# Performance work log

Measured on AMD Instinct MI355X. Metric: run time of the kernel, lower is better.

The kernel has to match this reference:

```python
import jax, jax.numpy as jnp
import numpy as np

D, NH, E, F = 768, 12, 4, 3072            # embed dim, heads, experts/group, expert ffn (4*D)
NBLK, DEPTH = 2, 6                        # MoE blocks, DiT depth
N_A, N_B, N_C = 64, 32, 192               # group token counts
MA, FH, TC = 32, 8, 7                     # max_agents, future_horizon, traj_channels
BATCH = 8
T_TRAJ = MA * FH                          # 256 trajectory tokens
TFREQ = 256                               # sinusoidal timestep embedding dim
HD = D // NH

def _ln(x):
    mu = jnp.mean(x, -1, keepdims=True)
    v = jnp.var(x, -1, keepdims=True)
    return (x - mu) * jax.lax.rsqrt(v + 1e-6)

def _heads(x):
    b, n, _ = x.shape
    return x.reshape(b, n, NH, HD).transpose(0, 2, 1, 3)

def _attn(q, k, v):
    s = jnp.einsum('bhqd,bhkd->bhqk', q, k) * (HD ** -0.5)
    p = jax.nn.softmax(s, -1)
    o = jnp.einsum('bhqk,bhkd->bhqd', p, v)
    b, h, n, d = o.shape
    return o.transpose(0, 2, 1, 3).reshape(b, n, h * d)

def _cross(q_in, kv_in, W):
    # W: [4, D, D] = (Wq, Wk, Wv, Wo)
    q = _heads(q_in @ W[0]); k = _heads(kv_in @ W[1]); v = _heads(kv_in @ W[2])
    return _attn(q, k, v) @ W[3]

def _moe(x, Wr, W1, W2):
    # top-1 switch routing: gate = softmax prob of selected expert
    gates = jax.nn.softmax(x @ Wr)                       # [B,N,E]
    idx = jnp.argmax(gates, -1)                          # [B,N]
    gval = jnp.take_along_axis(gates, idx[..., None], -1)  # [B,N,1]
    h = jax.nn.gelu(jnp.einsum('bnd,edf->bnef', x, W1))
    y = jnp.einsum('bnef,efd->bned', h, W2)
    sel = jax.nn.one_hot(idx, W1.shape[0], dtype=x.dtype) * gval
    return jnp.einsum('bned,bne->bnd', y, sel)

def _forward(x_traj, tokens_A, tokens_B, tokens_C, W_traj, b_traj, W_ftime,
             Wt1, bt1, Wt2, bt2, moe_attn_W, moe_router, moe_W1, moe_W2,
             dit_qkv, dit_qkv_b, dit_proj, dit_proj_b, dit_mlp1, dit_mlp1_b,
             dit_mlp2, dit_mlp2_b, dit_ada, dit_ada_b,
             out_ada_W, out_ada_b, out_W, out_b, t):
    B = x_traj.shape[0]
    # timestep conditioning (DiT TimestepEmbedder)
    half = TFREQ // 2
    freqs = jnp.exp(-np.log(10000.0) * jnp.arange(half, dtype=jnp.float32) / half)
    ang = t.astype(jnp.float32)[:, None] * freqs
    temb = jnp.concatenate([jnp.cos(ang), jnp.sin(ang)], -1)     # [B,TFREQ]
    c = jax.nn.silu(temb @ Wt1 + bt1) @ Wt2 + bt2                # [B,D]

    # trajectory embedding + future-time embedding
    traj = x_traj.reshape(B, T_TRAJ, TC) @ W_traj + b_traj       # [B,256,D]
    traj = traj + jnp.tile(W_ftime, (MA, 1))[None]

    # StackedMoEBlocks: directed cross-attn A->C->B + per-group top-1 expert routing
    a, bg, cg = tokens_A, tokens_B, tokens_C
    for i in range(NBLK):
        cg = cg + _cross(_ln(cg), a, moe_attn_W[i, 0])
        bg = bg + _cross(_ln(bg), cg, moe_attn_W[i, 1])
        a = a + _moe(_ln(a), moe_router[i, 0], moe_W1[i, 0], moe_W2[i, 0])
        bg = bg + _moe(_ln(bg), moe_router[i, 1], moe_W1[i, 1], moe_W2[i, 1])
        cg = cg + _moe(_ln(cg), moe_router[i, 2], moe_W1[i, 2], moe_W2[i, 2])

    # DiT backbone over [traj | A | B | C], adaLN-zero conditioning on c
    x = jnp.concatenate([traj, a, bg, cg], 1)                    # [B,544,D]
    for i in range(DEPTH):
        mod = (jax.nn.silu(c) @ dit_ada[i] + dit_ada_b[i]).reshape(B, 6, 1, D)
        s1, sc1, g1, s2, sc2, g2 = [mod[:, j] for j in range(6)]
        h = _ln(x) * (1 + sc1) + s1
        qkv = h @ dit_qkv[i] + dit_qkv_b[i]
        q, k, v = jnp.split(qkv, 3, -1)
        x = x + g1 * (_attn(_heads(q), _heads(k), _heads(v)) @ dit_proj[i] + dit_proj_b[i])
        h = _ln(x) * (1 + sc2) + s2
        x = x + g2 * (jax.nn.gelu(h @ dit_mlp1[i] + dit_mlp1_b[i]) @ dit_mlp2[i] + dit_mlp2_b[i])

    # output head: final adaLN + projection to noise(+sigma), trajectory tokens only
    shift, scale = jnp.split(jax.nn.silu(c) @ out_ada_W + out_ada_b, 2, -1)
    h = _ln(x) * (1 + scale[:, None]) + shift[:, None]
    out = h @ out_W + out_b
    return out[:, :T_TRAJ].reshape(B, MA, FH, 2 * TC)

def setup_inputs() -> dict:
    key = jax.random.key(0)
    ks = jax.random.split(key, 24)
    n = jax.random.normal
    s = 0.02
    return dict(
        x_traj=n(ks[0], (BATCH, MA, FH, TC), jnp.float32),
        t=jax.random.randint(ks[1], (BATCH,), 0, 50),
        tokens_A=n(ks[2], (BATCH, N_A, D), jnp.float32),
        tokens_B=n(ks[3], (BATCH, N_B, D), jnp.float32),
        tokens_C=n(ks[4], (BATCH, N_C, D), jnp.float32),
        W_traj=n(ks[5], (TC, D)) * s, b_traj=jnp.zeros((D,)),
        W_ftime=n(ks[6], (FH, D)) * s,
        Wt1=n(ks[7], (TFREQ, D)) * s, bt1=jnp.zeros((D,)),
        Wt2=n(ks[8], (D, D)) * s, bt2=jnp.zeros((D,)),
        moe_attn_W=n(ks[9], (NBLK, 2, 4, D, D)) * s,
        moe_router=n(ks[10], (NBLK, 3, D, E)) * s,
        moe_W1=n(ks[11], (NBLK, 3, E, D, F)) * s,
        moe_W2=n(ks[12], (NBLK, 3, E, F, D)) * s,
        dit_qkv=n(ks[13], (DEPTH, D, 3 * D)) * s, dit_qkv_b=jnp.zeros((DEPTH, 3 * D)),
        dit_proj=n(ks[14], (DEPTH, D, D)) * s, dit_proj_b=jnp.zeros((DEPTH, D)),
        dit_mlp1=n(ks[15], (DEPTH, D, 4 * D)) * s, dit_mlp1_b=jnp.zeros((DEPTH, 4 * D)),
        dit_mlp2=n(ks[16], (DEPTH, 4 * D, D)) * s, dit_mlp2_b=jnp.zeros((DEPTH, D)),
        dit_ada=n(ks[17], (DEPTH, D, 6 * D)) * s, dit_ada_b=jnp.zeros((DEPTH, 6 * D)),
        out_ada_W=n(ks[18], (D, 2 * D)) * s, out_ada_b=jnp.zeros((2 * D,)),
        out_W=n(ks[19], (D, 2 * TC)) * s, out_b=jnp.zeros((2 * TC,)),
    )

def reference(x_traj, t, tokens_A, tokens_B, tokens_C, W_traj, b_traj, W_ftime,
              Wt1, bt1, Wt2, bt2, moe_attn_W, moe_router, moe_W1, moe_W2,
              dit_qkv, dit_qkv_b, dit_proj, dit_proj_b, dit_mlp1, dit_mlp1_b,
              dit_mlp2, dit_mlp2_b, dit_ada, dit_ada_b,
              out_ada_W, out_ada_b, out_W, out_b):
    return _forward(x_traj, tokens_A, tokens_B, tokens_C, W_traj, b_traj, W_ftime,
                    Wt1, bt1, Wt2, bt2, moe_attn_W, moe_router, moe_W1, moe_W2,
                    dit_qkv, dit_qkv_b, dit_proj, dit_proj_b, dit_mlp1, dit_mlp1_b,
                    dit_mlp2, dit_mlp2_b, dit_ada, dit_ada_b,
                    out_ada_W, out_ada_b, out_W, out_b, t)
```

## Files before the change

kernel.cpp:

```cpp
#include <hip/hip_runtime.h>
#include <hip/hip_bf16.h>
#include <math.h>

#define D 768
#define NH 12
#define HD 64
#define NEXP 4
#define FF 3072
#define NBLK 2
#define DEPTH 6
#define NA 64
#define NB 32
#define NC 192
#define BATCH 8
#define TTRAJ 256
#define NTOK 544
#define MAXTOK 1536
#define MOER 2304

typedef __attribute__((ext_vector_type(8))) short short8v;
typedef __attribute__((ext_vector_type(4))) float f32x4;

__device__ __forceinline__ float siluf(float v) { return v / (1.f + expf(-v)); }
__device__ __forceinline__ float geluf(float v) {
    float u = 0.7978845608028654f * (v + 0.044715f * v * v * v);
    return 0.5f * v * (1.f + tanhf(u));
}
__device__ __forceinline__ unsigned short f2bf(float f) {
    union { float f; unsigned u; } v; v.f = f;
    unsigned r = v.u + 0x7fffu + ((v.u >> 16) & 1u);
    return (unsigned short)(r >> 16);
}
__device__ __forceinline__ float bf2f(unsigned short u) {
    union { unsigned u; float f; } v; v.u = ((unsigned)u) << 16; return v.f;
}
__device__ __forceinline__ void gl16(const unsigned short* g, unsigned short* l) {
    __builtin_amdgcn_global_load_lds(
        (const __attribute__((address_space(1))) void*)g,
        (__attribute__((address_space(3))) void*)l, 16, 0, 0);
}

__global__ void timestep_kernel(const int* __restrict__ t, unsigned short* __restrict__ tembP) {
    int i = blockIdx.x * blockDim.x + threadIdx.x;
    if (i >= 128 * 256) return;
    int b = i >> 8, j = i & 255;
    float v = 0.f;
    if (b < BATCH) {
        int jj = (j & 127);
        float freq = expf(-logf(10000.f) * (float)jj / 128.f);
        float ang = (float)t[b] * freq;
        v = (j < 128) ? cosf(ang) : sinf(ang);
    }
    tembP[i] = f2bf(v);
}

__global__ void add_ftime(float* __restrict__ traj, const float* __restrict__ wf, int total) {
    int i = blockIdx.x * blockDim.x + threadIdx.x;
    if (i >= total) return;
    int col = i % D;
    int n = (i / D) % TTRAJ;
    traj[i] += wf[(n & 7) * D + col];
}

__global__ void cvt_bf16(const float* __restrict__ in, unsigned short* __restrict__ out, int n8) {
    int i = blockIdx.x * blockDim.x + threadIdx.x;
    if (i >= n8) return;
    float4 a = *(const float4*)(in + i * 8);
    float4 b = *(const float4*)(in + i * 8 + 4);
    unsigned short t[8] = {f2bf(a.x), f2bf(a.y), f2bf(a.z), f2bf(a.w),
                           f2bf(b.x), f2bf(b.y), f2bf(b.z), f2bf(b.w)};
    *(short8v*)(out + i * 8) = *(short8v*)t;
}

template<int ACT>
__global__ __launch_bounds__(256) void gemm_act(
    const float* __restrict__ A, int lda,
    const float* __restrict__ B, int ldb,
    const float* __restrict__ bias,
    float* __restrict__ C, int ldc,
    int M, int N, int K)
{
    __shared__ float As[16][65];
    __shared__ float Bs[16][65];
    int tid = threadIdx.x;
    int tx = tid & 15, ty = tid >> 4;
    int row0 = blockIdx.y * 64, col0 = blockIdx.x * 64;
    float acc[4][4] = {};
    for (int k0 = 0; k0 < K; k0 += 16) {
        #pragma unroll
        for (int i = 0; i < 4; ++i) {
            int e = tid + 256 * i; int m = e >> 4; int kk = e & 15;
            int gr = row0 + m, gk = k0 + kk;
            As[kk][m] = (gr < M && gk < K) ? A[(size_t)gr * lda + gk] : 0.f;
        }
        #pragma unroll
        for (int i = 0; i < 4; ++i) {
            int e = tid + 256 * i; int kk = e >> 6; int n = e & 63;
            int gk = k0 + kk, gc = col0 + n;
            Bs[kk][n] = (gk < K && gc < N) ? B[(size_t)gk * ldb + gc] : 0.f;
        }
        __syncthreads();
        #pragma unroll
        for (int kk = 0; kk < 16; ++kk) {
            float a[4], bv[4];
            #pragma unroll
            for (int i = 0; i < 4; ++i) a[i] = As[kk][ty * 4 + i];
            #pragma unroll
            for (int j = 0; j < 4; ++j) bv[j] = Bs[kk][tx * 4 + j];
            #pragma unroll
            for (int i = 0; i < 4; ++i)
                #pragma unroll
                for (int j = 0; j < 4; ++j) acc[i][j] += a[i] * bv[j];
        }
        __syncthreads();
    }
    #pragma unroll
    for (int i = 0; i < 4; ++i) {
        int gr = row0 + ty * 4 + i; if (gr >= M) continue;
        #pragma unroll
        for (int j = 0; j < 4; ++j) {
            int gc = col0 + tx * 4 + j; if (gc >= N) continue;
            float v = acc[i][j] + (bias ? bias[gc] : 0.f);
            if (ACT == 1) v = siluf(v);
            if (ACT == 2) v = geluf(v);
            C[(size_t)gr * ldc + gc] = v;
        }
    }
}

__global__ __launch_bounds__(256) void transpose_cvt(
    const float* __restrict__ in, unsigned short* __restrict__ out, int K, int N)
{
    __shared__ unsigned short Ls[64][72];
    const float* src = in + (size_t)blockIdx.z * K * N;
    unsigned short* dst = out + (size_t)blockIdx.z * K * N;
    int k0 = blockIdx.y * 64, n0 = blockIdx.x * 64;
    int tid = threadIdx.x;
    int r = tid >> 2, c0 = (tid & 3) * 16;
    {
        const float* sp = src + (size_t)(k0 + r) * N + n0 + c0;
        #pragma unroll
        for (int j = 0; j < 16; j += 4) {
            float4 f = *(const float4*)(sp + j);
            Ls[c0 + j + 0][r] = f2bf(f.x);
            Ls[c0 + j + 1][r] = f2bf(f.y);
            Ls[c0 + j + 2][r] = f2bf(f.z);
            Ls[c0 + j + 3][r] = f2bf(f.w);
        }
    }
    __syncthreads();
    {
        unsigned short tmp[16];
        #pragma unroll
        for (int j = 0; j < 16; ++j) tmp[j] = Ls[r][c0 + j];
        unsigned short* dp = dst + (size_t)(n0 + r) * K + k0 + c0;
        *(short8v*)dp = *(short8v*)tmp;
        *(short8v*)(dp + 8) = *(short8v*)(tmp + 8);
    }
}

template<int ACT, int OUT, int TN, int TM>
__global__ __launch_bounds__(256) void gemm_lds(
    const unsigned short* __restrict__ A,
    const unsigned short* __restrict__ BT,
    const float* __restrict__ bias,
    float* __restrict__ Cf, unsigned short* __restrict__ Cb, int ldc,
    int K, int qscale_cols,
    const float* __restrict__ mod, int modstride, int gchunk, int ntok, int mrows,
    size_t bt_zs = 0, size_t bias_zs = 0, size_t c_zs = 0)
{
    constexpr int NCF = TN / 32;
    constexpr int NBS = TN / 64;
    constexpr int NMR = TM / 32;
    constexpr int NAI = TM / 64;
    constexpr int NST = (NAI > NBS) ? NAI : NBS;
    if (bt_zs) BT += (size_t)blockIdx.z * bt_zs;
    if (bias && bias_zs) bias += (size_t)blockIdx.z * bias_zs;
    if (c_zs) { if (Cf) Cf += (size_t)blockIdx.z * c_zs; if (Cb) Cb += (size_t)blockIdx.z * c_zs; }
    __shared__ unsigned short As[2][TM * 32];
    __shared__ unsigned short Bs[2][TN * 32];
    int tid = threadIdx.x, w = tid >> 6, lane = tid & 63;
    int row0 = blockIdx.y * TM, col0 = blockIdx.x * TN;
    int wrow = (w >> 1) * (TM / 2), wcol = (w & 1) * (TN / 2);
    int lr = lane & 15, g = lane >> 4;
    f32x4 acc[NMR][NCF] = {};

    int ra[NST], ka[NST], la[NST];
    #pragma unroll
    for (int i = 0; i < NST; ++i) {
        int off = tid * 16 + i * 4096;
        int row = off >> 6;
        int slot = (off >> 4) & 3;
        ra[i] = row;
        ka[i] = (slot ^ ((row >> 1) & 3)) * 8;
        la[i] = off >> 1;
    }
    int nt = K >> 5, cur = 0;
    #pragma unroll
    for (int i = 0; i < NAI; ++i)
        gl16(A + (size_t)(row0 + ra[i]) * K + ka[i], &As[0][la[i]]);
    #pragma unroll
    for (int i = 0; i < NBS; ++i)
        gl16(BT + (size_t)(col0 + ra[i]) * K + ka[i], &Bs[0][la[i]]);

    for (int t = 0; t < nt; ++t) {
        __syncthreads();
        if (t + 1 < nt) {
            int k0 = (t + 1) << 5;
            #pragma unroll
            for (int i = 0; i < NAI; ++i)
                gl16(A + (size_t)(row0 + ra[i]) * K + k0 + ka[i], &As[cur ^ 1][la[i]]);
            #pragma unroll
            for (int i = 0; i < NBS; ++i)
                gl16(BT + (size_t)(col0 + ra[i]) * K + k0 + ka[i], &Bs[cur ^ 1][la[i]]);
        }
        short8v av[NMR], bv[NCF];
        #pragma unroll
        for (int mr = 0; mr < NMR; ++mr) {
            int row = wrow + mr * 16 + lr;
            av[mr] = *(const short8v*)&As[cur][row * 32 + (g ^ ((row >> 1) & 3)) * 8];
        }
        #pragma unroll
        for (int nc = 0; nc < NCF; ++nc) {
            int row = wcol + nc * 16 + lr;
            bv[nc] = *(const short8v*)&Bs[cur][row * 32 + (g ^ ((row >> 1) & 3)) * 8];
        }
        #pragma unroll
        for (int mr = 0; mr < NMR; ++mr)
            #pragma unroll
            for (int nc = 0; nc < NCF; ++nc)
                acc[mr][nc] = __builtin_amdgcn_mfma_f32_16x16x32_bf16(
                    av[mr], bv[nc], acc[mr][nc], 0, 0, 0);
        cur ^= 1;
    }
    int rbase = g * 4;
    #pragma unroll
    for (int mr = 0; mr < NMR; ++mr) {
        #pragma unroll
        for (int nc = 0; nc < NCF; ++nc) {
            int gc = col0 + wcol + nc * 16 + lr;
            float bb = bias ? bias[gc] : 0.f;
            #pragma unroll
            for (int r = 0; r < 4; ++r) {
                int gr = row0 + wrow + mr * 16 + rbase + r;
                if (gr >= mrows) continue;
                float v = acc[mr][nc][r] + bb;
                if (ACT == 1) v = siluf(v);
                if (ACT == 2) v = geluf(v);
                if (OUT == 0) {
                    Cf[(size_t)gr * ldc + gc] = v;
                } else if (OUT == 1) {
                    if (gc < qscale_cols) v *= 0.125f;
                    Cb[(size_t)gr * ldc + gc] = f2bf(v);
                } else {
                    float gg = 1.f;
                    if (mod) gg = mod[(size_t)(gr / ntok) * modstride + gchunk * D + gc];
                    size_t idx = (size_t)gr * ldc + gc;
                    Cb[idx] = f2bf(bf2f(Cb[idx]) + gg * v);
                }
            }
        }
    }
}

template<int ACT>
__global__ __launch_bounds__(512, 4) void gemm_lds256(
    const unsigned short* __restrict__ A,
    const unsigned short* __restrict__ BT,
    const float* __restrict__ bias,
    unsigned short* __restrict__ Cb, int ldc,
    int K, int qscale_cols)
{
    __shared__ unsigned short As[2][256 * 32];
    __shared__ unsigned short Bs[2][128 * 32];
    int tid = threadIdx.x, w = tid >> 6, lane = tid & 63;
    int row0 = blockIdx.y * 256, col0 = blockIdx.x * 128;
    int wrow = (w >> 1) * 64, wcol = (w & 1) * 64;
    int lr = lane & 15, g = lane >> 4;
    f32x4 acc[4][4] = {};

    int ra[2], ka[2], la[2];
    #pragma unroll
    for (int i = 0; i < 2; ++i) {
        int off = tid * 16 + i * 8192;
        int row = off >> 6;
        int slot = (off >> 4) & 3;
        ra[i] = row;
        ka[i] = (slot ^ ((row >> 1) & 3)) * 8;
        la[i] = off >> 1;
    }
    int rb, kb, lb;
    {
        int off = tid * 16;
        int row = off >> 6;
        int slot = (off >> 4) & 3;
        rb = row;
        kb = (slot ^ ((row >> 1) & 3)) * 8;
        lb = off >> 1;
    }
    int nt = K >> 5, cur = 0;
    #pragma unroll
    for (int i = 0; i < 2; ++i)
        gl16(A + (size_t)(row0 + ra[i]) * K + ka[i], &As[0][la[i]]);
    gl16(BT + (size_t)(col0 + rb) * K + kb, &Bs[0][lb]);

    for (int t = 0; t < nt; ++t) {
        __syncthreads();
        if (t + 1 < nt) {
            int k0 = (t + 1) << 5;
            #pragma unroll
            for (int i = 0; i < 2; ++i)
                gl16(A + (size_t)(row0 + ra[i]) * K + k0 + ka[i], &As[cur ^ 1][la[i]]);
            gl16(BT + (size_t)(col0 + rb) * K + k0 + kb, &Bs[cur ^ 1][lb]);
        }
        short8v av[4], bv[4];
        #pragma unroll
        for (int mr = 0; mr < 4; ++mr) {
            int row = wrow + mr * 16 + lr;
            av[mr] = *(const short8v*)&As[cur][row * 32 + (g ^ ((row >> 1) & 3)) * 8];
        }
        #pragma unroll
        for (int nc = 0; nc < 4; ++nc) {
            int row = wcol + nc * 16 + lr;
            bv[nc] = *(const short8v*)&Bs[cur][row * 32 + (g ^ ((row >> 1) & 3)) * 8];
        }
        #pragma unroll
        for (int mr = 0; mr < 4; ++mr)
            #pragma unroll
            for (int nc = 0; nc < 4; ++nc)
                acc[mr][nc] = __builtin_amdgcn_mfma_f32_16x16x32_bf16(
                    av[mr], bv[nc], acc[mr][nc], 0, 0, 0);
        cur ^= 1;
    }
    int rbase = g * 4;
    #pragma unroll
    for (int mr = 0; mr < 4; ++mr) {
        #pragma unroll
        for (int nc = 0; nc < 4; ++nc) {
            int gc = col0 + wcol + nc * 16 + lr;
            float bb = bias ? bias[gc] : 0.f;
            #pragma unroll
            for (int r = 0; r < 4; ++r) {
                int gr = row0 + wrow + mr * 16 + rbase + r;
                float v = acc[mr][nc][r] + bb;
                if (ACT == 2) v = geluf(v);
                if (gc < qscale_cols) v *= 0.125f;
                Cb[(size_t)gr * ldc + gc] = f2bf(v);
            }
        }
    }
}

template<int PHASE>
__global__ __launch_bounds__(256) void moe_lds(
    const unsigned short* __restrict__ A,
    const unsigned short* __restrict__ BTconv,
    unsigned short* __restrict__ Cb,
    const int* __restrict__ cnt, const int* __restrict__ list,
    const float* __restrict__ gval, int RT, int egbase)
{
    constexpr int K  = (PHASE == 1) ? 768 : 3072;
    constexpr int TN = (PHASE == 1) ? 128 : 64;
    constexpr int NCF = TN / 32;
    constexpr int NBS = TN / 64;
    int egl = blockIdx.y / RT, rt = blockIdx.y % RT;
    int eg = egbase + egl;
    int c0 = cnt[eg];
    int mbase = rt * 128;
    if (mbase >= c0) return;
    int mcount = min(128, c0 - mbase);
    __shared__ int toks[128];
    int tid = threadIdx.x, w = tid >> 6, lane = tid & 63;
    if (tid < 128) toks[tid] = list[eg * MAXTOK + mbase + min(tid, mcount - 1)];
    __syncthreads();

    __shared__ unsigned short As[2][128 * 32];
    __shared__ unsigned short Bs[2][TN * 32];
    const unsigned short* BT = BTconv + (size_t)egl * (768 * 3072);
    int col0 = blockIdx.x * TN;
    int wrow = (w >> 1) * 64, wcol = (w & 1) * (TN / 2);
    int lr = lane & 15, g = lane >> 4;
    f32x4 acc[4][NCF] = {};

    int ra[2], ka[2], la[2], tok_s[2];
    #pragma unroll
    for (int i = 0; i < 2; ++i) {
        int off = tid * 16 + i * 4096;
        int row = off >> 6;
        int slot = (off >> 4) & 3;
        ra[i] = row;
        ka[i] = (slot ^ ((row >> 1) & 3)) * 8;
        la[i] = off >> 1;
        tok_s[i] = toks[row];
    }
    int nt = K >> 5, cur = 0;
    #pragma unroll
    for (int i = 0; i < 2; ++i)
        gl16(A + (size_t)tok_s[i] * K + ka[i], &As[0][la[i]]);
    #pragma unroll
    for (int i = 0; i < NBS; ++i)
        gl16(BT + (size_t)(col0 + ra[i]) * K + ka[i], &Bs[0][la[i]]);

    for (int t = 0; t < nt; ++t) {
        __syncthreads();
        if (t + 1 < nt) {
            int k0 = (t + 1) << 5;
            #pragma unroll
            for (int i = 0; i < 2; ++i)
                gl16(A + (size_t)tok_s[i] * K + k0 + ka[i], &As[cur ^ 1][la[i]]);
            #pragma unroll
            for (int i = 0; i < NBS; ++i)
                gl16(BT + (size_t)(col0 + ra[i]) * K + k0 + ka[i], &Bs[cur ^ 1][la[i]]);
        }
        short8v av[4], bv[NCF];
        #pragma unroll
        for (int mr = 0; mr < 4; ++mr) {
            int row = wrow + mr * 16 + lr;
            av[mr] = *(const short8v*)&As[cur][row * 32 + (g ^ ((row >> 1) & 3)) * 8];
        }
        #pragma unroll
        for (int nc = 0; nc < NCF; ++nc) {
            int row = wcol + nc * 16 + lr;
            bv[nc] = *(const short8v*)&Bs[cur][row * 32 + (g ^ ((row >> 1) & 3)) * 8];
        }
        #pragma unroll
        for (int mr = 0; mr < 4; ++mr)
            #pragma unroll
            for (int nc = 0; nc < NCF; ++nc)
                acc[mr][nc] = __builtin_amdgcn_mfma_f32_16x16x32_bf16(
                    av[mr], bv[nc], acc[mr][nc], 0, 0, 0);
        cur ^= 1;
    }
    int rbase = g * 4;
    #pragma unroll
    for (int mr = 0; mr < 4; ++mr) {
        #pragma unroll
        for (int r = 0; r < 4; ++r) {
            int m = wrow + mr * 16 + rbase + r;
            if (m >= mcount) continue;
            int tok = toks[m];
            #pragma unroll
            for (int nc = 0; nc < NCF; ++nc) {
                int gc = col0 + wcol + nc * 16 + lr;
                float v = acc[mr][nc][r];
                if (PHASE == 1) Cb[(size_t)tok * 3072 + gc] = f2bf(geluf(v));
                else {
                    size_t idx = (size_t)tok * 768 + gc;
                    Cb[idx] = f2bf(bf2f(Cb[idx]) + gval[tok] * v);
                }
            }
        }
    }
}

__global__ __launch_bounds__(256) void ln_kernel(
    const unsigned short* __restrict__ X, unsigned short* __restrict__ Y, int R, int ntok,
    const float* __restrict__ mod, int modstride, int shift_chunk, int scale_chunk)
{
    int r = blockIdx.x;
    if (r >= R) return;
    const unsigned short* xr = X + (size_t)r * D;
    int tid = threadIdx.x;
    int lane = tid & 63, wid = tid >> 6;
    float v0 = bf2f(xr[tid]), v1 = bf2f(xr[tid + 256]), v2 = bf2f(xr[tid + 512]);
    float s = v0 + v1 + v2;
    float s2 = v0 * v0 + v1 * v1 + v2 * v2;
    for (int off = 32; off > 0; off >>= 1) {
        s += __shfl_xor(s, off, 64);
        s2 += __shfl_xor(s2, off, 64);
    }
    __shared__ float shs[4], shs2[4];
    if (lane == 0) { shs[wid] = s; shs2[wid] = s2; }
    __syncthreads();
    float tot = shs[0] + shs[1] + shs[2] + shs[3];
    float tot2 = shs2[0] + shs2[1] + shs2[2] + shs2[3];
    float mu = tot * (1.f / 768.f);
    float var = tot2 * (1.f / 768.f) - mu * mu;
    float rs = rsqrtf(var + 1e-6f);
    int bb = r / ntok;
    float vv[3] = {v0, v1, v2};
    #pragma unroll
    for (int j = 0; j < 3; ++j) {
        int col = tid + j * 256;
        float nrm = (vv[j] - mu) * rs;
        float y = nrm;
        if (mod) {
            float scv = mod[(size_t)bb * modstride + scale_chunk * D + col];
            float shv = mod[(size_t)bb * modstride + shift_chunk * D + col];
            y = nrm * (1.f + scv) + shv;
        }
        Y[(size_t)r * D + col] = f2bf(y);
    }
}

__global__ __launch_bounds__(512) void attn_mfma(
    const unsigned short* __restrict__ Qp, int ldq, int qoff,
    const unsigned short* __restrict__ Kp, int ldk, int koff,
    const unsigned short* __restrict__ Vp, int ldv, int voff,
    unsigned short* __restrict__ O, int ldo,
    int Nq, int Nkv)
{
    __shared__ unsigned short Qs[128 * 64];
    __shared__ unsigned short Ks[64 * 64];
    __shared__ unsigned short Vs[64 * 64];
    __shared__ unsigned short Ps[128 * 64];
    int h = blockIdx.y, b = blockIdx.z, q0 = blockIdx.x * 128;
    int tid = threadIdx.x, w = tid >> 6, lane = tid & 63;
    int wrow = w * 16;
    int lr = lane & 15, g = lane >> 4;

    {
        int srow = tid >> 2, sc = (tid & 3) * 16;
        int gr = min(q0 + srow, Nq - 1);
        const unsigned short* qp = Qp + (size_t)(b * Nq + gr) * ldq + qoff + h * 64 + sc;
        short8v v0 = *(const short8v*)qp, v1 = *(const short8v*)(qp + 8);
        int s0 = sc >> 3;
        *(short8v*)&Qs[srow * 64 + (s0 ^ (srow & 7)) * 8] = v0;
        *(short8v*)&Qs[srow * 64 + ((s0 + 1) ^ (srow & 7)) * 8] = v1;
    }
    float m_r[4] = {-1e30f, -1e30f, -1e30f, -1e30f};
    float l_r[4] = {};
    f32x4 acc0 = {}, acc1 = {}, acc2 = {}, acc3 = {};

    for (int kv0 = 0; kv0 < Nkv; kv0 += 64) {
        {
            int t2 = tid & 255;
            int srow = t2 >> 2, sc = (t2 & 3) * 16;
            int gc = min(kv0 + srow, Nkv - 1);
            if (tid < 256) {
                const unsigned short* kp = Kp + (size_t)(b * Nkv + gc) * ldk + koff + h * 64 + sc;
                short8v v0 = *(const short8v*)kp, v1 = *(const short8v*)(kp + 8);
                int s0 = sc >> 3;
                *(short8v*)&Ks[srow * 64 + (s0 ^ (srow & 7)) * 8] = v0;
                *(short8v*)&Ks[srow * 64 + ((s0 + 1) ^ (srow & 7)) * 8] = v1;
            } else {
                const unsigned short* vp = Vp + (size_t)(b * Nkv + gc) * ldv + voff + h * 64 + sc;
                #pragma unroll
                for (int j = 0; j < 16; ++j) {
                    int d = sc + j;
                    Vs[d * 64 + (((srow >> 3) ^ (d & 7)) * 8) + (srow & 7)] = vp[j];
                }
            }
        }
        __syncthreads();
        short8v aq0, aq1;
        {
            int row = wrow + lr;
            aq0 = *(const short8v*)&Qs[row * 64 + ((0 + g) ^ (row & 7)) * 8];
            aq1 = *(const short8v*)&Qs[row * 64 + ((4 + g) ^ (row & 7)) * 8];
        }
        f32x4 sf[4];
        #pragma unroll
        for (int nc = 0; nc < 4; ++nc) {
            int row = nc * 16 + lr;
            short8v bk0 = *(const short8v*)&Ks[row * 64 + ((0 + g) ^ (row & 7)) * 8];
            short8v bk1 = *(const short8v*)&Ks[row * 64 + ((4 + g) ^ (row & 7)) * 8];
            f32x4 z = {};
            z = __builtin_amdgcn_mfma_f32_16x16x32_bf16(aq0, bk0, z, 0, 0, 0);
            sf[nc] = __builtin_amdgcn_mfma_f32_16x16x32_bf16(aq1, bk1, z, 0, 0, 0);
        }
        bool val0 = (kv0 + 0 * 16 + lr) < Nkv;
        bool val1 = (kv0 + 1 * 16 + lr) < Nkv;
        bool val2 = (kv0 + 2 * 16 + lr) < Nkv;
        bool val3 = (kv0 + 3 * 16 + lr) < Nkv;
        float fs[4];
        #pragma unroll
        for (int r = 0; r < 4; ++r) {
            float s0 = val0 ? sf[0][r] : -1e30f;
            float s1 = val1 ? sf[1][r] : -1e30f;
            float s2 = val2 ? sf[2][r] : -1e30f;
            float s3 = val3 ? sf[3][r] : -1e30f;
            float mx = fmaxf(fmaxf(s0, s1), fmaxf(s2, s3));
            mx = fmaxf(mx, __shfl_xor(mx, 1, 64));
            mx = fmaxf(mx, __shfl_xor(mx, 2, 64));
            mx = fmaxf(mx, __shfl_xor(mx, 4, 64));
            mx = fmaxf(mx, __shfl_xor(mx, 8, 64));
            float mn = fmaxf(m_r[r], mx);
            fs[r] = __expf(m_r[r] - mn);
            m_r[r] = mn;
            float p0 = __expf(s0 - mn), p1 = __expf(s1 - mn);
            float p2 = __expf(s2 - mn), p3 = __expf(s3 - mn);
            float rsum = p0 + p1 + p2 + p3;
            rsum += __shfl_xor(rsum, 1, 64);
            rsum += __shfl_xor(rsum, 2, 64);
            rsum += __shfl_xor(rsum, 4, 64);
            rsum += __shfl_xor(rsum, 8, 64);
            l_r[r] = l_r[r] * fs[r] + rsum;
            int ql = wrow + g * 4 + r;
            int base = ql * 64;
            int x7 = ql & 7;
            Ps[base + (((0 * 16 + lr) >> 3) ^ x7) * 8 + (lr & 7)] = f2bf(p0);
            Ps[base + (((1 * 16 + lr) >> 3) ^ x7) * 8 + (lr & 7)] = f2bf(p1);
            Ps[base + (((2 * 16 + lr) >> 3) ^ x7) * 8 + (lr & 7)] = f2bf(p2);
            Ps[base + (((3 * 16 + lr) >> 3) ^ x7) * 8 + (lr & 7)] = f2bf(p3);
            acc0[r] *= fs[r]; acc1[r] *= fs[r]; acc2[r] *= fs[r]; acc3[r] *= fs[r];
        }
        __syncthreads();
        short8v ap0, ap1;
        {
            int row = wrow + lr;
            ap0 = *(const short8v*)&Ps[row * 64 + ((0 + g) ^ (row & 7)) * 8];
            ap1 = *(const short8v*)&Ps[row * 64 + ((4 + g) ^ (row & 7)) * 8];
        }
        {
            int row = 0 * 16 + lr;
            short8v b0 = *(const short8v*)&Vs[row * 64 + ((0 + g) ^ (row & 7)) * 8];
            short8v b1 = *(const short8v*)&Vs[row * 64 + ((4 + g) ^ (row & 7)) * 8];
            acc0 = __builtin_amdgcn_mfma_f32_16x16x32_bf16(ap0, b0, acc0, 0, 0, 0);
            acc0 = __builtin_amdgcn_mfma_f32_16x16x32_bf16(ap1, b1, acc0, 0, 0, 0);
        }
        {
            int row = 1 * 16 + lr;
            short8v b0 = *(const short8v*)&Vs[row * 64 + ((0 + g) ^ (row & 7)) * 8];
            short8v b1 = *(const short8v*)&Vs[row * 64 + ((4 + g) ^ (row & 7)) * 8];
            acc1 = __builtin_amdgcn_mfma_f32_16x16x32_bf16(ap0, b0, acc1, 0, 0, 0);
            acc1 = __builtin_amdgcn_mfma_f32_16x16x32_bf16(ap1, b1, acc1, 0, 0, 0);
        }
        {
            int row = 2 * 16 + lr;
            short8v b0 = *(const short8v*)&Vs[row * 64 + ((0 + g) ^ (row & 7)) * 8];
            short8v b1 = *(const short8v*)&Vs[row * 64 + ((4 + g) ^ (row & 7)) * 8];
            acc2 = __builtin_amdgcn_mfma_f32_16x16x32_bf16(ap0, b0, acc2, 0, 0, 0);
            acc2 = __builtin_amdgcn_mfma_f32_16x16x32_bf16(ap1, b1, acc2, 0, 0, 0);
        }
        {
            int row = 3 * 16 + lr;
            short8v b0 = *(const short8v*)&Vs[row * 64 + ((0 + g) ^ (row & 7)) * 8];
            short8v b1 = *(const short8v*)&Vs[row * 64 + ((4 + g) ^ (row & 7)) * 8];
            acc3 = __builtin_amdgcn_mfma_f32_16x16x32_bf16(ap0, b0, acc3, 0, 0, 0);
            acc3 = __builtin_amdgcn_mfma_f32_16x16x32_bf16(ap1, b1, acc3, 0, 0, 0);
        }
        __syncthreads();
    }
    #pragma unroll
    for (int r = 0; r < 4; ++r) {
        int ql = wrow + g * 4 + r;
        if (q0 + ql >= Nq) continue;
        float rl = 1.f / l_r[r];
        unsigned short* op = O + (size_t)(b * Nq + q0 + ql) * ldo + h * 64 + lr;
        op[0]  = f2bf(acc0[r] * rl);
        op[16] = f2bf(acc1[r] * rl);
        op[32] = f2bf(acc2[r] * rl);
        op[48] = f2bf(acc3[r] * rl);
    }
}

__global__ __launch_bounds__(64) void router_kernel(
    const unsigned short* __restrict__ X, const float* __restrict__ WrBase,
    int* __restrict__ idx, float* __restrict__ gval)
{
    int tkn = blockIdx.x; int lane = threadIdx.x;
    int grp = (tkn >= 768) ? 2 : (tkn >= 512 ? 1 : 0);
    const float* Wr = WrBase + (size_t)grp * D * NEXP;
    const unsigned short* xr = X + (size_t)tkn * D;
    float p0 = 0, p1 = 0, p2 = 0, p3 = 0;
    for (int dd = lane; dd < D; dd += 64) {
        float xv = bf2f(xr[dd]);
        const float* wq = Wr + dd * 4;
        p0 += xv * wq[0]; p1 += xv * wq[1]; p2 += xv * wq[2]; p3 += xv * wq[3];
    }
    for (int off = 32; off > 0; off >>= 1) {
        p0 += __shfl_xor(p0, off, 64); p1 += __shfl_xor(p1, off, 64);
        p2 += __shfl_xor(p2, off, 64); p3 += __shfl_xor(p3, off, 64);
    }
    if (lane == 0) {
        float best = p0; int e = 0;
        if (p1 > best) { best = p1; e = 1; }
        if (p2 > best) { best = p2; e = 2; }
        if (p3 > best) { best = p3; e = 3; }
        float sum = expf(p0 - best) + expf(p1 - best) + expf(p2 - best) + expf(p3 - best);
        idx[tkn] = grp * 4 + e;
        gval[tkn] = 1.f / sum;
    }
}

__global__ __launch_bounds__(256) void scatter_kernel(
    const int* __restrict__ idx, int* __restrict__ cnt,
    int* __restrict__ list, int ntok)
{
    __shared__ int lcnt[12];
    int tid = threadIdx.x;
    if (tid < 12) lcnt[tid] = 0;
    __syncthreads();
    for (int i = tid; i < ntok; i += 256) {
        int e = idx[i];
        int pos = atomicAdd(&lcnt[e], 1);
        list[e * MAXTOK + pos] = i;
    }
    __syncthreads();
    if (tid < 12) cnt[tid] = lcnt[tid];
}

__global__ void concat_kernel(const float* __restrict__ traj, const unsigned short* __restrict__ a,
                              const unsigned short* __restrict__ bg, const unsigned short* __restrict__ cg,
                              unsigned short* __restrict__ x, int total)
{
    int i = blockIdx.x * blockDim.x + threadIdx.x;
    if (i >= total) return;
    int col = i % D;
    int r = i / D;
    int n = r % NTOK, b = r / NTOK;
    unsigned short v;
    if (n < 256)      v = f2bf(traj[((size_t)b * 256 + n) * D + col]);
    else if (n < 320) v = a[((size_t)b * 64 + (n - 256)) * D + col];
    else if (n < 352) v = bg[((size_t)b * 32 + (n - 320)) * D + col];
    else              v = cg[((size_t)b * 192 + (n - 352)) * D + col];
    x[i] = v;
}

__global__ void head_prep(const float* __restrict__ W, unsigned short* __restrict__ WT14) {
    int i = blockIdx.x * blockDim.x + threadIdx.x;
    if (i >= 14 * 768) return;
    int o = i / 768, d = i % 768;
    WT14[i] = f2bf(W[d * 14 + o]);
}

__global__ __launch_bounds__(64) void head_kernel(
    const unsigned short* __restrict__ lnb, const unsigned short* __restrict__ WT14,
    const float* __restrict__ bias, float* __restrict__ out)
{
    int r = blockIdx.x;
    int b = r >> 8, n = r & 255;
    const unsigned short* hrow = lnb + (size_t)(b * NTOK + n) * D;
    int l = threadIdx.x;
    if (l >= 56) return;
    int o = l >> 2, p = l & 3;
    const unsigned short* hp = hrow + p * 192;
    const unsigned short* wp = WT14 + o * 768 + p * 192;
    float acc = 0.f;
    for (int i = 0; i < 192; i += 8) {
        short8v hv = *(const short8v*)(hp + i);
        short8v wv = *(const short8v*)(wp + i);
        #pragma unroll
        for (int j = 0; j < 8; ++j)
            acc += bf2f((unsigned short)hv[j]) * bf2f((unsigned short)wv[j]);
    }
    acc += __shfl_xor(acc, 1, 64);
    acc += __shfl_xor(acc, 2, 64);
    if (p == 0) out[(size_t)r * 14 + o] = acc + bias[o];
}

static inline void tcvt(const float* W, unsigned short* WT, int K, int N, int z, hipStream_t s) {
    transpose_cvt<<<dim3(N / 64, K / 64, z), 256, 0, s>>>(W, WT, K, N);
}
static inline void g_bf(int act, const unsigned short* A, const unsigned short* BT,
                        const float* bias, unsigned short* C, int ldc,
                        int M, int N, int K, int qcols, hipStream_t s)
{
    if (M % 256 == 0 && N % 128 == 0 && N >= 2304) {
        dim3 g(N / 128, M / 256);
        if (act == 2) gemm_lds256<2><<<g, 512, 0, s>>>(A, BT, bias, C, ldc, K, qcols);
        else          gemm_lds256<0><<<g, 512, 0, s>>>(A, BT, bias, C, ldc, K, qcols);
        return;
    }
    bool small = (M <= 1536);
    if (N != 768) {
        if (small) {
            dim3 g(N / 128, M / 64);
            if (act == 2) gemm_lds<2, 1, 128, 64><<<g, 256, 0, s>>>(A, BT, bias, nullptr, C, ldc, K, qcols, nullptr, 0, 0, 1, 1 << 30);
            else          gemm_lds<0, 1, 128, 64><<<g, 256, 0, s>>>(A, BT, bias, nullptr, C, ldc, K, qcols, nullptr, 0, 0, 1, 1 << 30);
        } else {
            dim3 g(N / 128, M / 128);
            if (act == 2) gemm_lds<2, 1, 128, 128><<<g, 256, 0, s>>>(A, BT, bias, nullptr, C, ldc, K, qcols, nullptr, 0, 0, 1, 1 << 30);
            else          gemm_lds<0, 1, 128, 128><<<g, 256, 0, s>>>(A, BT, bias, nullptr, C, ldc, K, qcols, nullptr, 0, 0, 1, 1 << 30);
        }
    } else {
        if (small) {
            dim3 g(N / 64, M / 64);
            if (act == 2) gemm_lds<2, 1, 64, 64><<<g, 256, 0, s>>>(A, BT, bias, nullptr, C, ldc, K, qcols, nullptr, 0, 0, 1, 1 << 30);
            else          gemm_lds<0, 1, 64, 64><<<g, 256, 0, s>>>(A, BT, bias, nullptr, C, ldc, K, qcols, nullptr, 0, 0, 1, 1 << 30);
        } else {
            dim3 g(N / 64, M / 128);
            if (act == 2) gemm_lds<2, 1, 64, 128><<<g, 256, 0, s>>>(A, BT, bias, nullptr, C, ldc, K, qcols, nullptr, 0, 0, 1, 1 << 30);
            else          gemm_lds<0, 1, 64, 128><<<g, 256, 0, s>>>(A, BT, bias, nullptr, C, ldc, K, qcols, nullptr, 0, 0, 1, 1 << 30);
        }
    }
}
static inline void g_res(const unsigned short* A, const unsigned short* BT,
                         const float* bias, unsigned short* C, int ldc, int M, int N, int K,
                         const float* mod, int modstride, int gchunk, int ntok, hipStream_t s)
{
    if (M <= 1536) {
        dim3 g(N / 64, M / 64);
        gemm_lds<0, 2, 64, 64><<<g, 256, 0, s>>>(A, BT, bias, nullptr, C, ldc, K, 0, mod, modstride, gchunk, ntok, 1 << 30);
    } else {
        dim3 g(N / 64, M / 128);
        gemm_lds<0, 2, 64, 128><<<g, 256, 0, s>>>(A, BT, bias, nullptr, C, ldc, K, 0, mod, modstride, gchunk, ntok, 1 << 30);
    }
}

extern "C" void kernel_launch(void* const* d_in, const int* in_sizes, int n_in,
                              void* d_out, int out_size, void* d_ws, size_t ws_size,
                              hipStream_t stream)
{
    const float* x_traj   = (const float*)d_in[0];
    const int*   t_arr    = (const int*)d_in[1];
    const float* tokA     = (const float*)d_in[2];
    const float* tokB     = (const float*)d_in[3];
    const float* tokC     = (const float*)d_in[4];
    const float* W_traj   = (const float*)d_in[5];
    const float* b_traj   = (const float*)d_in[6];
    const float* W_ftime  = (const float*)d_in[7];
    const float* Wt1      = (const float*)d_in[8];
    const float* bt1      = (const float*)d_in[9];
    const float* Wt2      = (const float*)d_in[10];
    const float* bt2      = (const float*)d_in[11];
    const float* moe_attn = (const float*)d_in[12];
    const float* moe_rout = (const float*)d_in[13];
    const float* moe_W1   = (const float*)d_in[14];
    const float* moe_W2   = (const float*)d_in[15];
    const float* dit_qkv  = (const float*)d_in[16];
    const float* dit_qkvb = (const float*)d_in[17];
    const float* dit_proj = (const float*)d_in[18];
    const float* dit_projb= (const float*)d_in[19];
    const float* dit_mlp1 = (const float*)d_in[20];
    const float* dit_mlp1b= (const float*)d_in[21];
    const float* dit_mlp2 = (const float*)d_in[22];
    const float* dit_mlp2b= (const float*)d_in[23];
    const float* dit_ada  = (const float*)d_in[24];
    const float* dit_adab = (const float*)d_in[25];
    const float* out_adaW = (const float*)d_in[26];
    const float* out_adab = (const float*)d_in[27];
    const float* out_W    = (const float*)d_in[28];
    const float* out_b    = (const float*)d_in[29];
    float* out = (float*)d_out;
    float* ws = (float*)d_ws;

    const size_t o_cnt  = 14336;
    const size_t o_idx  = 14400;
    const size_t o_gval = 16704;
    const size_t o_list = 19008;
    const size_t o_traj = 66624;
    const size_t o_a    = 1639488;
    const size_t o_x    = 3408960;
    const size_t o_lnb  = 6751296;
    const size_t o_qkvb = 8422464;
    const size_t o_attnO= 13435968;
    const size_t o_h    = 15107136;
    const size_t o_wt   = 24151104;
    const size_t o_wt14 = 28869696;
    const size_t o_tembP= 28875072;
    const size_t o_ub   = 28891456;
    const size_t o_scb  = 28940608;
    const size_t o_mod  = o_traj;
    const size_t o_mod2 = o_traj + 221184;

    const size_t o_wqkv  = 29000000;
    const size_t o_wproj = 34308416;
    const size_t o_wmlp1 = 36077888;
    const size_t o_wmlp2 = 43155776;
    const size_t o_wada  = 50233664;
    const size_t o_wada2 = 60850496;
    const size_t o_wcross= 61440320;
    const size_t o_wmoe1 = 66158912;
    const size_t o_wmoe2 = 94470464;
    const bool bigw = ws_size >= (size_t)123000000 * 4;

    int* cnt_p  = (int*)(ws + o_cnt);
    int* idx_p  = (int*)(ws + o_idx);
    int* list_p = (int*)(ws + o_list);
    float* gval_p = ws + o_gval;
    unsigned short* abf  = (unsigned short*)(ws + o_a);
    unsigned short* bgbf = abf + 512 * 768;
    unsigned short* cgbf = abf + 768 * 768;
    unsigned short* xbf  = (unsigned short*)(ws + o_x);
    unsigned short* lnb  = (unsigned short*)(ws + o_lnb);
    unsigned short* qkvb = (unsigned short*)(ws + o_qkvb);
    unsigned short* attO = (unsigned short*)(ws + o_attnO);
    unsigned short* hbuf = (unsigned short*)(ws + o_h);
    unsigned short* wt   = (unsigned short*)(ws + o_wt);
    unsigned short* wt14 = (unsigned short*)(ws + o_wt14);
    unsigned short* tembP= (unsigned short*)(ws + o_tembP);
    unsigned short* ub   = (unsigned short*)(ws + o_ub);
    unsigned short* scb  = (unsigned short*)(ws + o_scb);
    unsigned short* wqkvS = (unsigned short*)(ws + o_wqkv);
    unsigned short* wprojS= (unsigned short*)(ws + o_wproj);
    unsigned short* wmlp1S= (unsigned short*)(ws + o_wmlp1);
    unsigned short* wmlp2S= (unsigned short*)(ws + o_wmlp2);
    unsigned short* wadaS = (unsigned short*)(ws + o_wada);
    unsigned short* wada2S= (unsigned short*)(ws + o_wada2);
    unsigned short* wcrossS=(unsigned short*)(ws + o_wcross);
    unsigned short* wmoe1S= (unsigned short*)(ws + o_wmoe1);
    unsigned short* wmoe2S= (unsigned short*)(ws + o_wmoe2);
    unsigned short* c_q  = qkvb;
    unsigned short* c_kv = qkvb + 1179648;

    const size_t WSZ = (size_t)D * D;

    gemm_act<0><<<dim3(12, 32), 256, 0, stream>>>(x_traj, 7, W_traj, D, b_traj,
                                                  ws + o_traj, D, BATCH * TTRAJ, D, 7);
    add_ftime<<<(BATCH * TTRAJ * D + 255) / 256, 256, 0, stream>>>(ws + o_traj, W_ftime, BATCH * TTRAJ * D);

    cvt_bf16<<<(512 * 768 / 8 + 255) / 256, 256, 0, stream>>>(tokA, abf, 512 * 768 / 8);
    cvt_bf16<<<(256 * 768 / 8 + 255) / 256, 256, 0, stream>>>(tokB, bgbf, 256 * 768 / 8);
    cvt_bf16<<<(1536 * 768 / 8 + 255) / 256, 256, 0, stream>>>(tokC, cgbf, 1536 * 768 / 8);
    head_prep<<<42, 256, 0, stream>>>(out_W, wt14);

    if (bigw) {
        tcvt(dit_qkv,  wqkvS,  D, 3 * D, DEPTH, stream);
        tcvt(dit_proj, wprojS, D, D, DEPTH, stream);
        tcvt(dit_mlp1, wmlp1S, D, FF, DEPTH, stream);
        tcvt(dit_mlp2, wmlp2S, FF, D, DEPTH, stream);
        tcvt(dit_ada,  wadaS,  D, 6 * D, DEPTH, stream);
        tcvt(out_adaW, wada2S, D, 2 * D, 1, stream);
        tcvt(moe_attn, wcrossS, D, D, NBLK * 2 * 4, stream);
        tcvt(moe_W1,   wmoe1S, D, FF, NBLK * 3 * NEXP, stream);
        tcvt(moe_W2,   wmoe2S, FF, D, NBLK * 3 * NEXP, stream);
    }

    timestep_kernel<<<128, 256, 0, stream>>>(t_arr, tembP);
    tcvt(Wt1, wt, 256, D, 1, stream);
    gemm_lds<1, 1, 64, 128><<<dim3(12, 1), 256, 0, stream>>>(
        tembP, wt, bt1, nullptr, ub, D, 256, 0, nullptr, 0, 0, 1, 128);
    tcvt(Wt2, wt, D, D, 1, stream);
    gemm_lds<1, 1, 64, 128><<<dim3(12, 1), 256, 0, stream>>>(
        ub, wt, bt2, nullptr, scb, D, D, 0, nullptr, 0, 0, 1, 128);

    for (int i = 0; i < NBLK; ++i) {
        {
            const unsigned short* Wc;
            if (bigw) Wc = wcrossS + (size_t)(i * 2 + 0) * 4 * WSZ;
            else { tcvt(moe_attn + (size_t)(i * 2 + 0) * 4 * WSZ, wt, D, D, 4, stream); Wc = wt; }
            ln_kernel<<<BATCH * NC, 256, 0, stream>>>(cgbf, lnb, BATCH * NC, 1, nullptr, 0, 0, 0);
            g_bf(0, lnb, Wc, nullptr, c_q, D, BATCH * NC, D, D, 768, stream);
            g_bf(0, abf, Wc + 1 * WSZ, nullptr, c_kv, 2 * D, BATCH * NA, 2 * D, D, 0, stream);
            attn_mfma<<<dim3((NC + 127) / 128, NH, BATCH), 512, 0, stream>>>(
                c_q, D, 0, c_kv, 2 * D, 0, c_kv, 2 * D, D, attO, D, NC, NA);
            g_res(attO, Wc + 3 * WSZ, nullptr, cgbf, D, BATCH * NC, D, D, nullptr, 0, 0, 1, stream);
        }
        {
            const unsigned short* Wc;
            if (bigw) Wc = wcrossS + (size_t)(i * 2 + 1) * 4 * WSZ;
            else { tcvt(moe_attn + (size_t)(i * 2 + 1) * 4 * WSZ, wt, D, D, 4, stream); Wc = wt; }
            ln_kernel<<<BATCH * NB, 256, 0, stream>>>(bgbf, lnb, BATCH * NB, 1, nullptr, 0, 0, 0);
            g_bf(0, lnb, Wc, nullptr, c_q, D, BATCH * NB, D, D, 768, stream);
            g_bf(0, cgbf, Wc + 1 * WSZ, nullptr, c_kv, 2 * D, BATCH * NC, 2 * D, D, 0, stream);
            attn_mfma<<<dim3(1, NH, BATCH), 512, 0, stream>>>(
                c_q, D, 0, c_kv, 2 * D, 0, c_kv, 2 * D, D, attO, D, NB, NC);
            g_res(attO, Wc + 3 * WSZ, nullptr, bgbf, D, BATCH * NB, D, D, nullptr, 0, 0, 1, stream);
        }
        ln_kernel<<<MOER, 256, 0, stream>>>(abf, lnb, MOER, 1, nullptr, 0, 0, 0);
        router_kernel<<<MOER, 64, 0, stream>>>(lnb, moe_rout + (size_t)(i * 3) * D * NEXP, idx_p, gval_p);
        scatter_kernel<<<1, 256, 0, stream>>>(idx_p, cnt_p, list_p, MOER);
        const int RT = 12;
        if (bigw) {
            moe_lds<1><<<dim3(24, 12 * RT), 256, 0, stream>>>(
                lnb, wmoe1S + (size_t)(i * 3) * NEXP * D * FF, hbuf,
                cnt_p, list_p, gval_p, RT, 0);
            moe_lds<2><<<dim3(12, 12 * RT), 256, 0, stream>>>(
                hbuf, wmoe2S + (size_t)(i * 3) * NEXP * D * FF, abf,
                cnt_p, list_p, gval_p, RT, 0);
        } else {
            for (int g = 0; g < 3; ++g) {
                tcvt(moe_W1 + (size_t)(i * 3 + g) * NEXP * D * FF, wt, D, FF, NEXP, stream);
                moe_lds<1><<<dim3(24, 4 * RT), 256, 0, stream>>>(
                    lnb, wt, hbuf, cnt_p, list_p, gval_p, RT, g * 4);
                tcvt(moe_W2 + (size_t)(i * 3 + g) * NEXP * FF * D, wt, FF, D, NEXP, stream);
                moe_lds<2><<<dim3(12, 4 * RT), 256, 0, stream>>>(
                    hbuf, wt, abf, cnt_p, list_p, gval_p, RT, g * 4);
            }
        }
    }

    concat_kernel<<<(BATCH * NTOK * D + 255) / 256, 256, 0, stream>>>(
        ws + o_traj, abf, bgbf, cgbf, xbf, BATCH * NTOK * D);

    if (bigw) {
        gemm_lds<0, 0, 128, 128><<<dim3(36, 1, DEPTH), 256, 0, stream>>>(
            scb, wadaS, dit_adab, ws + o_mod, nullptr, 6 * D, D, 0,
            nullptr, 0, 0, 1, 8,
            (size_t)D * 6 * D, (size_t)6 * D, (size_t)8 * 6 * D);
        gemm_lds<0, 0, 128, 128><<<dim3(12, 1), 256, 0, stream>>>(
            scb, wada2S, out_adab, ws + o_mod2, nullptr, 2 * D, D, 0, nullptr, 0, 0, 1, 8);
    } else {
        for (int i = 0; i < DEPTH; ++i) {
            tcvt(dit_ada + (size_t)i * D * 6 * D, wt, D, 6 * D, 1, stream);
            gemm_lds<0, 0, 128, 128><<<dim3(36, 1), 256, 0, stream>>>(
                scb, wt, dit_adab + (size_t)i * 6 * D, ws + o_mod + (size_t)i * 8 * 6 * D,
                nullptr, 6 * D, D, 0, nullptr, 0, 0, 1, 8);
        }
        tcvt(out_adaW, wt, D, 2 * D, 1, stream);
        gemm_lds<0, 0, 128, 128><<<dim3(12, 1), 256, 0, stream>>>(
            scb, wt, out_adab, ws + o_mod2, nullptr, 2 * D, D, 0, nullptr, 0, 0, 1, 8);
    }

    const int R = BATCH * NTOK;
    for (int i = 0; i < DEPTH; ++i) {
        const float* mod_l = ws + o_mod + (size_t)i * 8 * 6 * D;
        const unsigned short *Wq = nullptr, *Wp = nullptr, *Wm1 = nullptr, *Wm2 = nullptr;
        if (bigw) {
            Wq  = wqkvS  + (size_t)i * D * 3 * D;
            Wp  = wprojS + (size_t)i * D * D;
            Wm1 = wmlp1S + (size_t)i * D * FF;
            Wm2 = wmlp2S + (size_t)i * D * FF;
        }
        ln_kernel<<<R, 256, 0, stream>>>(xbf, lnb, R, NTOK, mod_l, 6 * D, 0, 1);
        if (!bigw) { tcvt(dit_qkv + (size_t)i * D * 3 * D, wt, D, 3 * D, 1, stream); Wq = wt; }
        g_bf(0, lnb, Wq, dit_qkvb + (size_t)i * 3 * D, qkvb, 3 * D, R, 3 * D, D, 768, stream);
        attn_mfma<<<dim3((NTOK + 127) / 128, NH, BATCH), 512, 0, stream>>>(
            qkvb, 3 * D, 0, qkvb, 3 * D, D, qkvb, 3 * D, 2 * D, attO, D, NTOK, NTOK);
        if (!bigw) { tcvt(dit_proj + (size_t)i * D * D, wt, D, D, 1, stream); Wp = wt; }
        g_res(attO, Wp, dit_projb + (size_t)i * D, xbf, D, R, D, D,
              mod_l, 6 * D, 2, NTOK, stream);
        ln_kernel<<<R, 256, 0, stream>>>(xbf, lnb, R, NTOK, mod_l, 6 * D, 3, 4);
        if (!bigw) { tcvt(dit_mlp1 + (size_t)i * D * FF, wt, D, FF, 1, stream); Wm1 = wt; }
        g_bf(2, lnb, Wm1, dit_mlp1b + (size_t)i * FF, hbuf, FF, R, FF, D, 0, stream);
        if (!bigw) { tcvt(dit_mlp2 + (size_t)i * FF * D, wt, FF, D, 1, stream); Wm2 = wt; }
        g_res(hbuf, Wm2, dit_mlp2b + (size_t)i * D, xbf, D, R, D, FF,
              mod_l, 6 * D, 5, NTOK, stream);
    }

    ln_kernel<<<R, 256, 0, stream>>>(xbf, lnb, R, NTOK, ws + o_mod2, 2 * D, 0, 1);
    head_kernel<<<BATCH * TTRAJ, 64, 0, stream>>>(lnb, wt14, out_b, out);
}
```

Before: 2.270 ms.

## Split-K the MoE down-projection with atomic fp32 scratch and a finalize pass

Replaces the MoE second expert GEMM (K=3072) with a split-K version that splits K into four chunks across blockIdx.z. Partial sums go into a zeroed fp32 scratch buffer through atomicAdd, and a separate kernel applies the gate and adds the result into the bf16 residual. The aim is more parallelism for the sparse per-expert tiles, which were too few blocks to fill the GPU. In exchange it adds two extra launches, atomic traffic and a scratch buffer that aliases the qkv workspace.

```diff
diff --git a/kernel.cpp b/kernel.cpp
--- a/kernel.cpp
+++ b/kernel.cpp
@@ -70,6 +70,26 @@
     unsigned short t[8] = {f2bf(a.x), f2bf(a.y), f2bf(a.z), f2bf(a.w),
                            f2bf(b.x), f2bf(b.y), f2bf(b.z), f2bf(b.w)};
     *(short8v*)(out + i * 8) = *(short8v*)t;
+}
+
+__global__ void zero_f32(float* __restrict__ p, int n4) {
+    int i = blockIdx.x * blockDim.x + threadIdx.x;
+    if (i < n4) *(float4*)(p + (size_t)i * 4) = make_float4(0.f, 0.f, 0.f, 0.f);
+}
+
+__global__ void moe_fin(const float* __restrict__ scr, const float* __restrict__ gval,
+                        unsigned short* __restrict__ abf, int total4) {
+    int i = blockIdx.x * blockDim.x + threadIdx.x;
+    if (i >= total4) return;
+    size_t base = (size_t)i * 4;
+    int tok = (int)(base / 768);
+    float g = gval[tok];
+    float4 s = *(const float4*)(scr + base);
+    unsigned short* p = abf + base;
+    p[0] = f2bf(bf2f(p[0]) + g * s.x);
+    p[1] = f2bf(bf2f(p[1]) + g * s.y);
+    p[2] = f2bf(bf2f(p[2]) + g * s.z);
+    p[3] = f2bf(bf2f(p[3]) + g * s.w);
 }
 
 template<int ACT>
@@ -448,6 +468,96 @@
                     size_t idx = (size_t)tok * 768 + gc;
                     Cb[idx] = f2bf(bf2f(Cb[idx]) + gval[tok] * v);
                 }
+            }
+        }
+    }
+}
+
+__global__ __launch_bounds__(256) void moe_lds2k(
+    const unsigned short* __restrict__ A,
+    const unsigned short* __restrict__ BTconv,
+    float* __restrict__ scr,
+    const int* __restrict__ cnt, const int* __restrict__ list, int RT)
+{
+    constexpr int K = 3072;
+    constexpr int TN = 64;
+    constexpr int NCF = 2;
+    int egl = blockIdx.y / RT, rt = blockIdx.y % RT;
+    int c0 = cnt[egl];
+    int mbase = rt * 128;
+    if (mbase >= c0) return;
+    int mcount = min(128, c0 - mbase);
+    __shared__ int toks[128];
+    int tid = threadIdx.x, w = tid >> 6, lane = tid & 63;
+    if (tid < 128) toks[tid] = list[egl * MAXTOK + mbase + min(tid, mcount - 1)];
+    __syncthreads();
+
+    __shared__ unsigned short As[2][128 * 32];
+    __shared__ unsigned short Bs[2][TN * 32];
+    const unsigned short* BT = BTconv + (size_t)egl * (768 * 3072);
+    int col0 = blockIdx.x * TN;
+    int ksbase = blockIdx.z * 768;
+    int wrow = (w >> 1) * 64, wcol = (w & 1) * (TN / 2);
+    int lr = lane & 15, g = lane >> 4;
+    f32x4 acc[4][NCF] = {};
+
+    int ra[2], ka[2], la[2], tok_s[2];
+    #pragma unroll
+    for (int i = 0; i < 2; ++i) {
+        int off = tid * 16 + i * 4096;
+        int row = off >> 6;
+        int slot = (off >> 4) & 3;
+        ra[i] = row;
+        ka[i] = (slot ^ ((row >> 1) & 3)) * 8;
+        la[i] = off >> 1;
+        tok_s[i] = toks[row];
+    }
+    int nt = 768 >> 5, cur = 0;
+    #pragma unroll
+    for (int i = 0; i < 2; ++i)
+        gl16(A + (size_t)tok_s[i] * K + ksbase + ka[i], &As[0][la[i]]);
+    gl16(BT + (size_t)(col0 + ra[0]) * K + ksbase + ka[0], &Bs[0][la[0]]);
+
+    for (int t = 0; t < nt; ++t) {
+        __syncthreads();
+        if (t + 1 < nt) {
+            int k0 = ksbase + ((t + 1) << 5);
+            #pragma unroll
+            for (int i = 0; i < 2; ++i)
+                gl16(A + (size_t)tok_s[i] * K + k0 + ka[i], &As[cur ^ 1][la[i]]);
+            gl16(BT + (size_t)(col0 + ra[0]) * K + k0 + ka[0], &Bs[cur ^ 1][la[0]]);
+        }
+        short8v av[4], bv[NCF];
+        #pragma unroll
+        for (int mr = 0; mr < 4; ++mr) {
+            int row = wrow + mr * 16 + lr;
+            av[mr] = *(const short8v*)&As[cur][row * 32 + (g ^ ((row >> 1) & 3)) * 8];
+        }
+        #pragma unroll
+        for (int nc = 0; nc < NCF; ++nc) {
+            int row = wcol + nc * 16 + lr;
+            bv[nc] = *(const short8v*)&Bs[cur][row * 32 + (g ^ ((row >> 1) & 3)) * 8];
+        }
+        #pragma unroll
+        for (int mr = 0; mr < 4; ++mr)
+            #pragma unroll
+            for (int nc = 0; nc < NCF; ++nc)
+                acc[mr][nc] = __builtin_amdgcn_mfma_f32_16x16x32_bf16(
+                    av[mr], bv[nc], acc[mr][nc], 0, 0, 0);
+        cur ^= 1;
+    }
+    int rbase = g * 4;
+    #pragma unroll
+    for (int mr = 0; mr < 4; ++mr) {
+        #pragma unroll
+        for (int r = 0; r < 4; ++r) {
+            int m = wrow + mr * 16 + rbase + r;
+            if (m >= mcount) continue;
+            int tok = toks[m];
+            #pragma unroll
+            for (int nc = 0; nc < NCF; ++nc) {
+                int gc = col0 + wcol + nc * 16 + lr;
+                atomicAdd(&scr[(size_t)tok * 768 + gc], acc[mr][nc][r]);
             }
         }
     }
@@ -884,6 +994,7 @@
     unsigned short* wmoe2S= (unsigned short*)(ws + o_wmoe2);
     unsigned short* c_q  = qkvb;
     unsigned short* c_kv = qkvb + 1179648;
+    float* scr = ws + o_qkvb;
 
     const size_t WSZ = (size_t)D * D;
 
@@ -947,9 +1058,11 @@
             moe_lds<1><<<dim3(24, 12 * RT), 256, 0, stream>>>(
                 lnb, wmoe1S + (size_t)(i * 3) * NEXP * D * FF, hbuf,
                 cnt_p, list_p, gval_p, RT, 0);
-            moe_lds<2><<<dim3(12, 12 * RT), 256, 0, stream>>>(
-                hbuf, wmoe2S + (size_t)(i * 3) * NEXP * D * FF, abf,
-                cnt_p, list_p, gval_p, RT, 0);
+            zero_f32<<<(442368 + 255) / 256, 256, 0, stream>>>(scr, 442368);
+            moe_lds2k<<<dim3(12, 12 * RT, 4), 256, 0, stream>>>(
+                hbuf, wmoe2S + (size_t)(i * 3) * NEXP * D * FF, scr,
+                cnt_p, list_p, RT);
+            moe_fin<<<(442368 + 255) / 256, 256, 0, stream>>>(scr, gval_p, abf, 442368);
         } else {
             for (int g = 0; g < 3; ++g) {
                 tcvt(moe_W1 + (size_t)(i * 3 + g) * NEXP * D * FF, wt, D, FF, NEXP, stream);
```

New measurement: 2.230 ms. About the same (-1.8%).
